# Optimization experiments

Hardware: AMD Instinct MI355X
Metric: run time of the kernel (lower is better)

## Reference

```python
import jax, jax.numpy as jnp
import numpy as np

B, T, K = 64, 4096, 48  # batch, seq_len, n_tags


def setup_inputs() -> dict:
    key = jax.random.key(0)
    k1, k2, k3 = jax.random.split(key, 3)
    labels = jax.random.randint(k1, (B, T), 0, K)
    y_true = jax.nn.one_hot(labels, K, dtype=jnp.float32)  # one-hot targets, per dense_loss docstring
    y_pred = jax.random.normal(k2, (B, T, K), dtype=jnp.float32)  # emission scores
    trans = jax.random.normal(k3, (K, K), dtype=jnp.float32) * 0.1  # transition matrix (glorot-ish scale)
    return {"y_true": y_true, "y_pred": y_pred, "trans": trans}


def reference(y_true, y_pred, trans):
    # mask: positions where all emission scores > -1e6 (padding marker)
    mask = jnp.all(y_pred > -1e6, axis=2, keepdims=True).astype(y_pred.dtype)  # (B,T,1)
    y_true = y_true * mask
    y_pred = y_pred * mask

    # target_score: per-label emission score + transition score of the true path
    point_score = jnp.einsum('bni,bni->b', y_true, y_pred)
    trans_score = jnp.einsum('bni,ij,bnj->b', y_true[:, :-1], trans, y_true[:, 1:])
    target = point_score + trans_score  # (B,)

    # log_norm_step recurrence (CRF forward algorithm), fused as a single scan
    init = y_pred[:, 0]  # (B,K)
    xs = jnp.swapaxes(y_pred[:, 1:], 0, 1)  # (T-1,B,K)
    ms = jnp.swapaxes(mask[:, 1:], 0, 1)    # (T-1,B,1)

    def step(s, xm):
        x, m = xm
        # logsumexp over previous-tag axis: s (B,K_prev) + trans (K_prev,K_cur)
        new = jax.scipy.special.logsumexp(s[:, :, None] + trans[None, :, :], axis=1) + x
        s = m * new + (1.0 - m) * s
        return s, None

    s_final, _ = jax.lax.scan(step, init, (xs, ms))
    log_norm = jax.scipy.special.logsumexp(s_final, axis=1)  # (B,)

    # dense_loss returns log_norm - target_score (negative log-likelihood per example)
    return log_norm - target
```

## Files before the change

kernel.cpp:

```cpp
#include <hip/hip_runtime.h>

#define BB 64
#define TT 4096
#define KK 48
#define UST 56
#define PST 56
#define WS_LS_OFF 16384
#define WS_U_OFF 32768
#define SEGBYTES 6144

typedef __bf16 bf16_t;
typedef bf16_t bf16x8 __attribute__((ext_vector_type(8)));
typedef float f32x4 __attribute__((ext_vector_type(4)));
typedef float f32x16 __attribute__((ext_vector_type(16)));

__device__ __forceinline__ float fexp(float x) {
    return __builtin_amdgcn_exp2f(x * 1.4426950408889634f);
}
__device__ __forceinline__ float flog2(float x) { return __builtin_amdgcn_logf(x); }
__device__ __forceinline__ float rdlanef(float v, int l) {
    return __int_as_float(__builtin_amdgcn_readlane(__float_as_int(v), l));
}
__device__ __forceinline__ unsigned int bf16bits(float f) {
    return (unsigned int)__builtin_bit_cast(unsigned short, (bf16_t)f);
}
__device__ __forceinline__ float bf2f(bf16_t h) {
    return __uint_as_float(((unsigned int)__builtin_bit_cast(unsigned short, h)) << 16);
}
__device__ __forceinline__ unsigned int pktrunc(float lo, float hi) {
    return __builtin_amdgcn_perm(__float_as_uint(hi), __float_as_uint(lo), 0x07060302u);
}

__global__ __launch_bounds__(256) void fused_kernel(
    const float* __restrict__ y_true, const float* __restrict__ y_pred,
    const float* __restrict__ trans, float* __restrict__ ws_target,
    int* __restrict__ ws_ls, bf16_t* __restrict__ ws_u, int nseg) {
    const int s = blockIdx.x, b = blockIdx.y;
    const int seglen = TT / nseg;
    const int nch = seglen / 64;
    const int tid = threadIdx.x;
    const int w = tid >> 6;
    const int lane = tid & 63;
    const int q = lane >> 4;
    const int n = lane & 15;
    const int ncol = 16 * w + n;

    __shared__ __align__(16) float4 exf[64 * 13];
    __shared__ __align__(16) bf16_t Ubuf[48 * UST + 16];
    __shared__ unsigned long long pb;
    __shared__ int lsb[4];

    bf16x8 afrag[3][2];
    if (w < 3) {
#pragma unroll
        for (int mt = 0; mt < 3; mt++) {
#pragma unroll
            for (int ks = 0; ks < 2; ks++) {
                bf16x8 f;
#pragma unroll
                for (int j = 0; j < 8; j++) {
                    int k = 32 * ks + 8 * q + j;
                    float v = (k < KK) ? fexp(trans[k * KK + 16 * mt + n]) : 0.0f;
                    f[j] = (bf16_t)v;
                }
                afrag[mt][ks] = f;
            }
        }
    }

    {
        uint4* p = (uint4*)Ubuf;
        for (int i = tid; i < (48 * UST + 16) / 8; i += 256) p[i] = make_uint4(0, 0, 0, 0);
    }
    __syncthreads();
    if (tid < KK) Ubuf[tid * UST + tid] = (bf16_t)1.0f;

    const bf16_t* bptr0 = &Ubuf[ncol * UST + 8 * q];
    const bf16_t* bptr1 = &Ubuf[ncol * UST + 32 + 8 * q];
    bf16_t* wp0 = &Ubuf[ncol * UST + 0 + 4 * q];
    bf16_t* wp1 = &Ubuf[ncol * UST + 16 + 4 * q];
    bf16_t* wp2 = &Ubuf[ncol * UST + 32 + 4 * q];

    f32x4 z4 = {0.0f, 0.0f, 0.0f, 0.0f};
    int ls = 0;
    int cnt = 0;
    float sc_acc = 0.0f;

    for (int ch = 0; ch < nch; ch++) {
        __syncthreads();
        if (w == 3) {
            const int t0c = s * seglen + ch * 64;
            const size_t rowbase = ((size_t)b * TT + t0c + lane) * KK;
            const float4* yp4 = (const float4*)(y_pred + rowbase);
            const float4* yt4 = (const float4*)(y_true + rowbase);
            float dot = 0.0f, labf = 0.0f, pmin = 1e30f;
            float4* exrow = &exf[lane * 13];
#pragma unroll 4
            for (int g = 0; g < 12; g++) {
                float4 p = yp4[g];
                float4 a = yt4[g];
                dot = fmaf(a.x, p.x, fmaf(a.y, p.y, fmaf(a.z, p.z, fmaf(a.w, p.w, dot))));
                float e0 = (float)(4 * g);
                labf = fmaf(a.x, e0, fmaf(a.y, e0 + 1.0f, fmaf(a.z, e0 + 2.0f, fmaf(a.w, e0 + 3.0f, labf))));
                pmin = fminf(pmin, fminf(fminf(p.x, p.y), fminf(p.z, p.w)));
                exrow[g] = make_float4(fexp(p.x), fexp(p.y), fexp(p.z), fexp(p.w));
            }
            bool mt_ok = pmin > -1e6f;
            unsigned long long bal = __ballot(mt_ok);
            if (lane == 0) pb = bal;

            float labB = 0.0f, pmB = 1e30f;
            const bool hasB = (t0c + 64 < TT);
            if (hasB && lane < 12) {
                const size_t bdbase = ((size_t)b * TT + t0c + 64) * KK;
                float4 a = ((const float4*)(y_true + bdbase))[lane];
                float4 p = ((const float4*)(y_pred + bdbase))[lane];
                float e0 = (float)(4 * lane);
                labB = fmaf(a.x, e0, fmaf(a.y, e0 + 1.0f, fmaf(a.z, e0 + 2.0f, a.w * (e0 + 3.0f))));
                pmB = fminf(fminf(p.x, p.y), fminf(p.z, p.w));
            }
#pragma unroll
            for (int off = 1; off < 16; off <<= 1) {
                labB += __shfl_xor(labB, off);
                pmB = fminf(pmB, __shfl_xor(pmB, off));
            }
            int labB_i = (int)(rdlanef(labB, 0) + 0.5f);
            float mB = (hasB && rdlanef(pmB, 0) > -1e6f) ? 1.0f : 0.0f;

            int labt = (int)(labf + 0.5f);
            float mft = mt_ok ? 1.0f : 0.0f;
            int lnx = __shfl(labt, (lane + 1) & 63);
            float mnx = __shfl(mft, (lane + 1) & 63);
            if (lane == 63) { lnx = labB_i; mnx = mB; }
            sc_acc += mft * dot + mft * mnx * trans[labt * KK + lnx];
        }
        __syncthreads();
        if (w < 3) {
            const unsigned long long mk = pb;
            const int tt0 = (s == 0 && ch == 0) ? 1 : 0;
            for (int tt = tt0; tt < 64; tt++) {
                if (!((mk >> tt) & 1ull)) continue;

                bf16x8 bf0 = __builtin_bit_cast(bf16x8, *(const uint4*)bptr0);
                bf16x8 bf1 = __builtin_bit_cast(bf16x8, *(const uint4*)bptr1);

                f32x4 acc0 = __builtin_amdgcn_mfma_f32_16x16x32_bf16(afrag[0][0], bf0, z4, 0, 0, 0);
                acc0 = __builtin_amdgcn_mfma_f32_16x16x32_bf16(afrag[0][1], bf1, acc0, 0, 0, 0);
                f32x4 acc1 = __builtin_amdgcn_mfma_f32_16x16x32_bf16(afrag[1][0], bf0, z4, 0, 0, 0);
                acc1 = __builtin_amdgcn_mfma_f32_16x16x32_bf16(afrag[1][1], bf1, acc1, 0, 0, 0);
                f32x4 acc2 = __builtin_amdgcn_mfma_f32_16x16x32_bf16(afrag[2][0], bf0, z4, 0, 0, 0);
                acc2 = __builtin_amdgcn_mfma_f32_16x16x32_bf16(afrag[2][1], bf1, acc2, 0, 0, 0);

                float4 ex0 = exf[tt * 13 + q];
                float4 ex1 = exf[tt * 13 + 4 + q];
                float4 ex2 = exf[tt * 13 + 8 + q];

                if (++cnt >= 6) {
                    float v00 = rdlanef(acc0[0], 0);
                    int k = (int)(__float_as_uint(v00) >> 23) - 127;
                    float r = __uint_as_float((unsigned int)(127 - k) << 23);
                    ls += k;
                    ex0.x *= r; ex0.y *= r; ex0.z *= r; ex0.w *= r;
                    ex1.x *= r; ex1.y *= r; ex1.z *= r; ex1.w *= r;
                    ex2.x *= r; ex2.y *= r; ex2.z *= r; ex2.w *= r;
                    cnt = 0;
                }

                *(uint2*)wp0 = make_uint2(pktrunc(acc0[0] * ex0.x, acc0[1] * ex0.y),
                                          pktrunc(acc0[2] * ex0.z, acc0[3] * ex0.w));
                *(uint2*)wp1 = make_uint2(pktrunc(acc1[0] * ex1.x, acc1[1] * ex1.y),
                                          pktrunc(acc1[2] * ex1.z, acc1[3] * ex1.w));
                *(uint2*)wp2 = make_uint2(pktrunc(acc2[0] * ex2.x, acc2[1] * ex2.y),
                                          pktrunc(acc2[2] * ex2.z, acc2[3] * ex2.w));
            }
        }
    }

    if (w == 3) {
#pragma unroll
        for (int off = 32; off; off >>= 1) sc_acc += __shfl_xor(sc_acc, off);
        if (lane == 0) ws_target[b * nseg + s] = sc_acc;
    }

    if (w < 3 && lane == 0) lsb[w] = ls;
    __syncthreads();
    if (w < 3 && lane < KK) {
        const int dl = ls - lsb[0];
        bf16_t* Uo = ws_u + (size_t)(b * nseg + s) * 3072;
        unsigned int wd[8];
#pragma unroll
        for (int j = 0; j < 8; j++) {
            float f0 = ldexpf(bf2f(Ubuf[(16 * w + 2 * j) * UST + lane]), dl);
            float f1 = ldexpf(bf2f(Ubuf[(16 * w + 2 * j + 1) * UST + lane]), dl);
            wd[j] = bf16bits(f0) | (bf16bits(f1) << 16);
        }
        *(uint4*)(Uo + (size_t)lane * 64 + 16 * w) = make_uint4(wd[0], wd[1], wd[2], wd[3]);
        *(uint4*)(Uo + (size_t)lane * 64 + 16 * w + 8) = make_uint4(wd[4], wd[5], wd[6], wd[7]);
    }
    if (tid == 0) ws_ls[b * nseg + s] = lsb[0];
}

__device__ __forceinline__ int chain_product(const bf16_t* __restrict__ A, bf16_t* Ub, int lane) {
    const int half = lane >> 5;
    const int l31 = lane & 31;
    f32x16 z16;
#pragma unroll
    for (int r = 0; r < 16; r++) z16[r] = 0.0f;

    bf16x8 af[2][3];
#pragma unroll
    for (int mt = 0; mt < 2; mt++) {
        int m = l31 + 32 * mt;
#pragma unroll
        for (int ks = 0; ks < 3; ks++) {
            if (m < KK)
                af[mt][ks] = __builtin_bit_cast(bf16x8, *(const uint4*)&A[(size_t)m * 64 + 16 * ks + 8 * half]);
            else
                af[mt][ks] = __builtin_bit_cast(bf16x8, make_uint4(0, 0, 0, 0));
        }
    }
    bf16x8 bg[3][2];
#pragma unroll
    for (int ks = 0; ks < 3; ks++)
#pragma unroll
        for (int nt = 0; nt < 2; nt++)
            bg[ks][nt] = __builtin_bit_cast(bf16x8, *(const uint4*)&Ub[(l31 + 32 * nt) * PST + 16 * ks + 8 * half]);

    f32x16 acc[4];
#pragma unroll
    for (int mt = 0; mt < 2; mt++)
#pragma unroll
        for (int nt = 0; nt < 2; nt++) {
            f32x16 a0 = __builtin_amdgcn_mfma_f32_32x32x16_bf16(af[mt][0], bg[0][nt], z16, 0, 0, 0);
            a0 = __builtin_amdgcn_mfma_f32_32x32x16_bf16(af[mt][1], bg[1][nt], a0, 0, 0, 0);
            acc[mt * 2 + nt] = __builtin_amdgcn_mfma_f32_32x32x16_bf16(af[mt][2], bg[2][nt], a0, 0, 0, 0);
        }

    float v00 = rdlanef(acc[0][0], 0);
    int k = (int)(__float_as_uint(v00) >> 23) - 127;
    float r = __uint_as_float((unsigned int)(127 - k) << 23);

#pragma unroll
    for (int mt = 0; mt < 2; mt++)
#pragma unroll
        for (int nt = 0; nt < 2; nt++) {
            int c = l31 + 32 * nt;
#pragma unroll
            for (int g = 0; g < 4; g++) {
                int a0 = 32 * mt + 8 * g + 4 * half;
                if (a0 < KK) {
                    const f32x16& Aq = acc[mt * 2 + nt];
                    unsigned int u0 = bf16bits(Aq[4 * g + 0] * r) | (bf16bits(Aq[4 * g + 1] * r) << 16);
                    unsigned int u1 = bf16bits(Aq[4 * g + 2] * r) | (bf16bits(Aq[4 * g + 3] * r) << 16);
                    *(uint2*)&Ub[c * PST + a0] = make_uint2(u0, u1);
                }
            }
        }
    return k;
}

__device__ __forceinline__ int chain_product_ldsA(const bf16_t* As, bf16_t* Ub, int lane) {
    const int half = lane >> 5;
    const int l31 = lane & 31;
    f32x16 z16;
#pragma unroll
    for (int r = 0; r < 16; r++) z16[r] = 0.0f;

    bf16x8 af[2][3];
#pragma unroll
    for (int mt = 0; mt < 2; mt++) {
        int m = l31 + 32 * mt;
#pragma unroll
        for (int ks = 0; ks < 3; ks++) {
            bf16x8 f;
#pragma unroll
            for (int j = 0; j < 8; j++) {
                int k = 16 * ks + 8 * half + j;
                f[j] = (m < KK) ? As[k * PST + m] : (bf16_t)0.0f;
            }
            af[mt][ks] = f;
        }
    }
    bf16x8 bg[3][2];
#pragma unroll
    for (int ks = 0; ks < 3; ks++)
#pragma unroll
        for (int nt = 0; nt < 2; nt++)
            bg[ks][nt] = __builtin_bit_cast(bf16x8, *(const uint4*)&Ub[(l31 + 32 * nt) * PST + 16 * ks + 8 * half]);

    f32x16 acc[4];
#pragma unroll
    for (int mt = 0; mt < 2; mt++)
#pragma unroll
        for (int nt = 0; nt < 2; nt++) {
            f32x16 a0 = __builtin_amdgcn_mfma_f32_32x32x16_bf16(af[mt][0], bg[0][nt], z16, 0, 0, 0);
            a0 = __builtin_amdgcn_mfma_f32_32x32x16_bf16(af[mt][1], bg[1][nt], a0, 0, 0, 0);
            acc[mt * 2 + nt] = __builtin_amdgcn_mfma_f32_32x32x16_bf16(af[mt][2], bg[2][nt], a0, 0, 0, 0);
        }

    float v00 = rdlanef(acc[0][0], 0);
    int k = (int)(__float_as_uint(v00) >> 23) - 127;
    float r = __uint_as_float((unsigned int)(127 - k) << 23);

#pragma unroll
    for (int mt = 0; mt < 2; mt++)
#pragma unroll
        for (int nt = 0; nt < 2; nt++) {
            int c = l31 + 32 * nt;
#pragma unroll
            for (int g = 0; g < 4; g++) {
                int a0 = 32 * mt + 8 * g + 4 * half;
                if (a0 < KK) {
                    const f32x16& Aq = acc[mt * 2 + nt];
                    unsigned int u0 = bf16bits(Aq[4 * g + 0] * r) | (bf16bits(Aq[4 * g + 1] * r) << 16);
                    unsigned int u1 = bf16bits(Aq[4 * g + 2] * r) | (bf16bits(Aq[4 * g + 3] * r) << 16);
                    *(uint2*)&Ub[c * PST + a0] = make_uint2(u0, u1);
                }
            }
        }
    return k;
}

__global__ __launch_bounds__(256) void phaseAB_kernel(
    const float* __restrict__ y_pred, const bf16_t* __restrict__ ws_u,
    const int* __restrict__ ws_ls, const float* __restrict__ ws_target,
    float* __restrict__ out, int nseg) {
    const int b = blockIdx.x;
    const int tid = threadIdx.x;
    const int w = tid >> 6;
    const int lane = tid & 63;
    const int per = nseg / 4;

    __shared__ __align__(16) bf16_t Ws[4][64 * PST];
    __shared__ int lsw[4];

    const int base = b * nseg + w * per;
    const bf16_t* s0 = ws_u + (size_t)base * 3072;
    for (int k = 0; k < KK; k++)
        Ws[w][lane * PST + k] = (lane < KK) ? s0[(size_t)k * 64 + lane] : (bf16_t)0.0f;
    int lsk = ws_ls[base];
    for (int j = 1; j < per; j++) {
        const bf16_t* A = ws_u + (size_t)(base + j) * 3072;
        lsk += ws_ls[base + j];
        lsk += chain_product(A, Ws[w], lane);
    }
    if (lane == 0) lsw[w] = lsk;
    __syncthreads();

    if (w == 0) {
        int ls2 = 0;
#pragma unroll
        for (int j = 1; j < 4; j++) ls2 += chain_product_ldsA(Ws[j], Ws[0], lane);

        float L = (float)(lsw[0] + lsw[1] + lsw[2] + lsw[3] + ls2);

        float x0 = (lane < KK) ? y_pred[(size_t)b * TT * KK + lane] : 0.0f;
        bool ok0 = (lane >= KK) || (x0 > -1e6f);
        bool m0 = (__ballot(ok0) == ~0ull);
        float xeff = (lane < KK) ? (m0 ? x0 : 0.0f) : 0.0f;
        float c0 = rdlanef(xeff, 0);
        float q0 = (lane < KK) ? fexp(xeff - c0) : 0.0f;

        float p = 0.0f;
        if (lane < KK) {
            for (int c = 0; c < KK; c++) {
                float qc = rdlanef(q0, c);
                p = fmaf(bf2f(Ws[0][c * PST + lane]), qc, p);
            }
        }
#pragma unroll
        for (int off = 32; off; off >>= 1) p += __shfl_xor(p, off);

        float tg = (lane < nseg) ? ws_target[b * nseg + lane] : 0.0f;
#pragma unroll
        for (int off = 32; off; off >>= 1) tg += __shfl_xor(tg, off);

        if (lane == 0) {
            out[b] = c0 + 0.6931471805599453f * (L + flog2(p)) - tg;
        }
    }
}

extern "C" void kernel_launch(void* const* d_in, const int* in_sizes, int n_in,
                              void* d_out, int out_size, void* d_ws, size_t ws_size,
                              hipStream_t stream) {
    const float* y_true = (const float*)d_in[0];
    const float* y_pred = (const float*)d_in[1];
    const float* trans = (const float*)d_in[2];
    float* out = (float*)d_out;

    int nseg = 16;
    if (ws_size >= (size_t)WS_U_OFF + (size_t)BB * 64 * SEGBYTES) nseg = 64;
    else if (ws_size >= (size_t)WS_U_OFF + (size_t)BB * 32 * SEGBYTES) nseg = 32;

    float* ws_target = (float*)d_ws;
    int* ws_ls = (int*)((char*)d_ws + WS_LS_OFF);
    bf16_t* ws_u = (bf16_t*)((char*)d_ws + WS_U_OFF);

    fused_kernel<<<dim3(nseg, BB), 256, 0, stream>>>(
        y_true, y_pred, trans, ws_target, ws_ls, ws_u, nseg);
    phaseAB_kernel<<<BB, 256, 0, stream>>>(y_pred, ws_u, ws_ls, ws_target, out, nseg);
}
```

Measured before the change: 269.2 us.

## Split segment-matrix reduction into parallel fold-by-8 kernel plus final tree reduction

Segment transfer-matrix products were previously reduced in a single 64-block kernel, where each wave serially chained nseg/4 matrices. A new fold8 kernel runs one block per group of 8 segments per batch row and reduces each group as a tree, writing the product back to the workspace. The final kernel then combines only nseg/8 partials. This exposes more parallelism and shortens the serial chain, at the cost of an extra kernel launch and a workspace round trip.

Measured after the change: 272.0 us. Within noise of the previous version (+1.1%).

```diff
diff --git a/kernel.cpp b/kernel.cpp
--- a/kernel.cpp
+++ b/kernel.cpp
@@ -321,38 +321,90 @@
     return k;
 }
 
-__global__ __launch_bounds__(256) void phaseAB_kernel(
+__global__ __launch_bounds__(256) void fold8_kernel(
+    bf16_t* __restrict__ ws_u, int* __restrict__ ws_ls, int nseg) {
+    const int s8 = blockIdx.x, b = blockIdx.y;
+    const int tid = threadIdx.x;
+    const int w = tid >> 6, lane = tid & 63;
+    const int base = b * nseg + s8 * 8;
+
+    __shared__ __align__(16) bf16_t Ws[4][64 * PST];
+    __shared__ int lsp[8];
+
+    {
+        const bf16_t* sE = ws_u + (size_t)(base + 2 * w) * 3072;
+        for (int k = 0; k < KK; k++)
+            Ws[w][lane * PST + k] = (lane < KK) ? sE[(size_t)k * 64 + lane] : (bf16_t)0.0f;
+        int lsk = ws_ls[base + 2 * w] + ws_ls[base + 2 * w + 1];
+        lsk += chain_product(ws_u + (size_t)(base + 2 * w + 1) * 3072, Ws[w], lane);
+        if (lane == 0) lsp[w] = lsk;
+    }
+    __syncthreads();
+    int k1 = 0;
+    if (w == 0) k1 = chain_product_ldsA(Ws[1], Ws[0], lane);
+    if (w == 2) {
+        int k2 = chain_product_ldsA(Ws[3], Ws[2], lane);
+        if (lane == 0) lsp[5] = k2;
+    }
+    __syncthreads();
+    if (w == 0) {
+        int k3 = chain_product_ldsA(Ws[2], Ws[0], lane);
+        if (lane < KK) {
+            bf16_t* Uo = ws_u + (size_t)base * 3072;
+            unsigned int wd[24];
+#pragma unroll
+            for (int j = 0; j < 24; j++) {
+                unsigned int lo = (unsigned int)__builtin_bit_cast(unsigned short, Ws[0][(2 * j) * PST + lane]);
+                unsigned int hi = (unsigned int)__builtin_bit_cast(unsigned short, Ws[0][(2 * j + 1) * PST + lane]);
+                wd[j] = lo | (hi << 16);
+            }
+#pragma unroll
+            for (int g = 0; g < 6; g++)
+                *(uint4*)(Uo + (size_t)lane * 64 + 8 * g) =
+                    make_uint4(wd[4 * g], wd[4 * g + 1], wd[4 * g + 2], wd[4 * g + 3]);
+        }
+        if (lane == 0)
+            ws_ls[base] = lsp[0] + lsp[1] + lsp[2] + lsp[3] + k1 + lsp[5] + k3;
+    }
+}
+
+__global__ __launch_bounds__(256) void final_kernel(
     const float* __restrict__ y_pred, const bf16_t* __restrict__ ws_u,
     const int* __restrict__ ws_ls, const float* __restrict__ ws_target,
     float* __restrict__ out, int nseg) {
     const int b = blockIdx.x;
     const int tid = threadIdx.x;
-    const int w = tid >> 6;
-    const int lane = tid & 63;
-    const int per = nseg / 4;
+    const int w = tid >> 6, lane = tid & 63;
+    const int npart = nseg / 8;
 
     __shared__ __align__(16) bf16_t Ws[4][64 * PST];
-    __shared__ int lsw[4];
-
-    const int base = b * nseg + w * per;
-    const bf16_t* s0 = ws_u + (size_t)base * 3072;
-    for (int k = 0; k < KK; k++)
-        Ws[w][lane * PST + k] = (lane < KK) ? s0[(size_t)k * 64 + lane] : (bf16_t)0.0f;
-    int lsk = ws_ls[base];
-    for (int j = 1; j < per; j++) {
-        const bf16_t* A = ws_u + (size_t)(base + j) * 3072;
-        lsk += ws_ls[base + j];
-        lsk += chain_product(A, Ws[w], lane);
-    }
-    if (lane == 0) lsw[w] = lsk;
+    __shared__ int lsp[8];
+    if (tid < 8) lsp[tid] = 0;
+    __syncthreads();
+
+    if (2 * w < npart) {
+        const int slotE = b * nseg + 16 * w;
+        const int slotL = slotE + 8;
+        const bf16_t* sE = ws_u + (size_t)slotE * 3072;
+        for (int k = 0; k < KK; k++)
+            Ws[w][lane * PST + k] = (lane < KK) ? sE[(size_t)k * 64 + lane] : (bf16_t)0.0f;
+        int lsk = ws_ls[slotE] + ws_ls[slotL];
+        lsk += chain_product(ws_u + (size_t)slotL * 3072, Ws[w], lane);
+        if (lane == 0) lsp[w] = lsk;
+    }
+    __syncthreads();
+    int k1 = 0;
+    if (npart >= 4 && w == 0) k1 = chain_product_ldsA(Ws[1], Ws[0], lane);
+    if (npart == 8 && w == 2) {
+        int k2 = chain_product_ldsA(Ws[3], Ws[2], lane);
+        if (lane == 0) lsp[5] = k2;
+    }
     __syncthreads();
 
     if (w == 0) {
-        int ls2 = 0;
-#pragma unroll
-        for (int j = 1; j < 4; j++) ls2 += chain_product_ldsA(Ws[j], Ws[0], lane);
-
-        float L = (float)(lsw[0] + lsw[1] + lsw[2] + lsw[3] + ls2);
+        int k3 = 0;
+        if (npart == 8) k3 = chain_product_ldsA(Ws[2], Ws[0], lane);
+        float L = (float)(lsp[0] + lsp[1] + lsp[2] + lsp[3] + k1 + lsp[5] + k3);
 
         float x0 = (lane < KK) ? y_pred[(size_t)b * TT * KK + lane] : 0.0f;
         bool ok0 = (lane >= KK) || (x0 > -1e6f);
@@ -399,5 +451,6 @@
 
     fused_kernel<<<dim3(nseg, BB), 256, 0, stream>>>(
         y_true, y_pred, trans, ws_target, ws_ls, ws_u, nseg);
-    phaseAB_kernel<<<BB, 256, 0, stream>>>(y_pred, ws_u, ws_ls, ws_target, out, nseg);
-}
+    fold8_kernel<<<dim3(nseg / 8, BB), 256, 0, stream>>>(ws_u, ws_ls, nseg);
+    final_kernel<<<BB, 256, 0, stream>>>(y_pred, ws_u, ws_ls, ws_target, out, nseg);
+}
```
